# Kernel tuning notes

Measured on AMD Instinct MI355X. Metric: run time of the kernel, lower is better.

## Reference

```python
import jax, jax.numpy as jnp
import numpy as np

EPS = 1e-06
TOP_K = 2


def setup_inputs() -> dict:
    key = jax.random.key(0)
    k1, k2 = jax.random.split(key)
    B, S, H, E = 4, 4096, 2048, 64
    x = jax.random.normal(k1, (B, S, H), dtype=jnp.float32)
    per_dim_scale = jnp.ones((H,), dtype=jnp.float32)
    W = jax.random.normal(k2, (H, E), dtype=jnp.float32) * 0.02  # Dense kernel [H, E]
    return {"x": x, "per_dim_scale": per_dim_scale, "W": W}


def reference(x, per_dim_scale, W):
    H = x.shape[-1]
    x_flat = x.reshape(-1, H)  # [T, H]
    # Parameter-free RMSNorm (Gemma4VNorm)
    normed = x_flat * jax.lax.rsqrt(jnp.mean(jnp.square(x_flat), axis=-1, keepdims=True) + EPS)
    # scale by 1/sqrt(H), then learnable per-dim scale
    normed = normed * jnp.asarray(H, normed.dtype) ** -0.5
    normed = normed * per_dim_scale.astype(normed.dtype)
    router_logits = normed @ W  # [T, E]
    router_probs = jax.nn.softmax(router_logits.astype(jnp.float32), axis=-1).astype(x.dtype)
    top_k_probs, top_k_indices = jax.lax.top_k(router_probs, TOP_K)  # [T, k]
    denom = jnp.maximum(jnp.sum(top_k_probs, axis=-1, keepdims=True),
                        jnp.asarray(1e-09, top_k_probs.dtype))
    top_k_probs = top_k_probs / denom
    # Sparse dispatch weights [T, E] (sum of scaled one-hots == scatter-add)
    T = router_probs.shape[0]
    rows = jnp.arange(T)[:, None]  # [T, 1] broadcast against [T, k]
    dispatch_weights = jnp.zeros_like(router_probs).at[rows, top_k_indices].add(top_k_probs)
    return dispatch_weights
```

## Files before the change

kernel.cpp:

```cpp
#include <hip/hip_runtime.h>
#include <math.h>

#define H 2048
#define E 64
#define TAU 1e-6f

#define MT 16
#define NST 4

#define RB 16
#define CB 512
#define NCH (H / CB)
#define PITCH 516

#define WHI_OFF 65792u
#define WFRAG_BYTES 262144u
#define WLO_OFF (WHI_OFF + WFRAG_BYTES)
#define WS_NEEDED ((size_t)(WLO_OFF + WFRAG_BYTES))

typedef __attribute__((ext_vector_type(8))) short short8;
typedef __attribute__((ext_vector_type(4))) float f32x4;

__device__ __forceinline__ unsigned short bf16_rne(float f) {
    unsigned u = __float_as_uint(f);
    unsigned r = u + 0x7fffu + ((u >> 16) & 1u);
    return (unsigned short)(r >> 16);
}

__global__ __launch_bounds__(256)
void prep_w(const float* __restrict__ Wm, int* __restrict__ flags,
            unsigned short* __restrict__ whi, unsigned short* __restrict__ wlo)
{
    const int tid = blockIdx.x * 256 + threadIdx.x;
    if (tid == 0) flags[0] = 0;
    const int lane = tid & 63;
    const int fb   = tid >> 6;
    const int kc   = fb >> 2;
    const int n    = fb & 3;
    const int r0   = kc * 32 + (lane >> 4) * 8;
    const int col  = n * 16 + (lane & 15);

    short8 hv, lv;
#pragma unroll
    for (int j = 0; j < 8; ++j) {
        const float w = Wm[(r0 + j) * E + col];
        const unsigned short hb = bf16_rne(w);
        const float hf = __uint_as_float((unsigned)hb << 16);
        const unsigned short lb = bf16_rne(w - hf);
        hv[j] = (short)hb;
        lv[j] = (short)lb;
    }
    *(short8*)(whi + (size_t)tid * 8) = hv;
    *(short8*)(wlo + (size_t)tid * 8) = lv;
}

__global__ __launch_bounds__(256, 2)
void router_nb(const float* __restrict__ x,
               const float* __restrict__ pds,
               const unsigned short* __restrict__ whi,
               const unsigned short* __restrict__ wlo,
               float* __restrict__ out,
               int* __restrict__ flags)
{
    __shared__ __align__(16) unsigned short ybuf[4][2][4][520];
    __shared__ float ssbuf[64];
    __shared__ float sfac[16];

    const int t    = threadIdx.x;
    const int wid  = t >> 6;
    const int lane = t & 63;
    const int lgrp = lane >> 4;
    const int lsub = lane & 15;
    const int row0 = blockIdx.x * MT;

    const int kcl_w  = lsub >> 2;
    const int koff_w = (lsub & 3) * 8;
    const int kbase  = wid * 512;

    f32x4 acc[4] = {{0.f,0.f,0.f,0.f},{0.f,0.f,0.f,0.f},
                    {0.f,0.f,0.f,0.f},{0.f,0.f,0.f,0.f}};
    float sq[4] = {0.f, 0.f, 0.f, 0.f};

    float4 xv[4][2];
#pragma unroll
    for (int rr = 0; rr < 4; ++rr) {
        const float* p = x + (size_t)(row0 + rr * 4 + lgrp) * H + kbase + lsub * 8;
        xv[rr][0] = *(const float4*)p;
        xv[rr][1] = *(const float4*)(p + 4);
    }

    for (int st = 0; st < NST; ++st) {
        const float* pb = pds + kbase + st * 128 + lsub * 8;
        const float4 p0 = *(const float4*)pb;
        const float4 p1 = *(const float4*)(pb + 4);
#pragma unroll
        for (int rr = 0; rr < 4; ++rr) {
            const float4 a0 = xv[rr][0];
            const float4 a1 = xv[rr][1];
            sq[rr] += a0.x * a0.x + a0.y * a0.y + a0.z * a0.z + a0.w * a0.w
                    + a1.x * a1.x + a1.y * a1.y + a1.z * a1.z + a1.w * a1.w;
            const float y[8] = { a0.x * p0.x, a0.y * p0.y, a0.z * p0.z, a0.w * p0.w,
                                 a1.x * p1.x, a1.y * p1.y, a1.z * p1.z, a1.w * p1.w };
            short8 hv, lv;
#pragma unroll
            for (int e = 0; e < 8; ++e) {
                const unsigned short hb = bf16_rne(y[e]);
                const unsigned short lb = bf16_rne(y[e] - __uint_as_float((unsigned)hb << 16));
                hv[e] = (short)hb;
                lv[e] = (short)lb;
            }
            const int didx = (rr * 4 + lgrp) * 32 + koff_w;
            *(short8*)(&ybuf[wid][0][kcl_w][didx]) = hv;
            *(short8*)(&ybuf[wid][1][kcl_w][didx]) = lv;
        }

        if (st + 1 < NST) {
#pragma unroll
            for (int rr = 0; rr < 4; ++rr) {
                const float* p = x + (size_t)(row0 + rr * 4 + lgrp) * H
                               + kbase + (st + 1) * 128 + lsub * 8;
                xv[rr][0] = *(const float4*)p;
                xv[rr][1] = *(const float4*)(p + 4);
            }
        }

        const int aoff = lsub * 32 + lgrp * 8;
#pragma unroll
        for (int kcl = 0; kcl < 4; ++kcl) {
            const int kc = wid * 16 + st * 4 + kcl;
            const unsigned short* wbh = whi + (size_t)kc * 2048 + lane * 8;
            const unsigned short* wbl = wlo + (size_t)kc * 2048 + lane * 8;
            short8 bh[4], bl[4];
#pragma unroll
            for (int n = 0; n < 4; ++n) {
                bh[n] = *(const short8*)(wbh + n * 512);
                bl[n] = *(const short8*)(wbl + n * 512);
            }
            const short8 ah = *(const short8*)(&ybuf[wid][0][kcl][aoff]);
            const short8 al = *(const short8*)(&ybuf[wid][1][kcl][aoff]);
#pragma unroll
            for (int n = 0; n < 4; ++n) {
                acc[n] = __builtin_amdgcn_mfma_f32_16x16x32_bf16(ah, bh[n], acc[n], 0, 0, 0);
                acc[n] = __builtin_amdgcn_mfma_f32_16x16x32_bf16(ah, bl[n], acc[n], 0, 0, 0);
                acc[n] = __builtin_amdgcn_mfma_f32_16x16x32_bf16(al, bh[n], acc[n], 0, 0, 0);
            }
        }
    }

    float* lb = (float*)ybuf;
    float* lw = lb + wid * 2080;
#pragma unroll
    for (int n = 0; n < 4; ++n)
#pragma unroll
        for (int q = 0; q < 4; ++q)
            lw[(lgrp * 4 + q) * 64 + n * 16 + lsub] = acc[n][q];

#pragma unroll
    for (int rr = 0; rr < 4; ++rr) {
        float s = sq[rr];
        s += __shfl_xor(s, 1);
        s += __shfl_xor(s, 2);
        s += __shfl_xor(s, 4);
        s += __shfl_xor(s, 8);
        if (lsub == 0) ssbuf[wid * 16 + rr * 4 + lgrp] = s;
    }
    __syncthreads();

    if (t < 16) {
        const float tot = ssbuf[t] + ssbuf[16 + t] + ssbuf[32 + t] + ssbuf[48 + t];
        sfac[t] = rsqrtf(tot * (1.0f / (float)H) + 1e-6f) * 0.022097086912079608f;
    }
    __syncthreads();

#pragma unroll
    for (int rr = 0; rr < 4; ++rr) {
        const int r = wid * 4 + rr;
        const float L = (lb[r * 64 + lane]        + lb[2080 + r * 64 + lane]
                       + lb[4160 + r * 64 + lane] + lb[6240 + r * 64 + lane]) * sfac[r];

        float m = L;
#pragma unroll
        for (int off = 32; off >= 1; off >>= 1)
            m = fmaxf(m, __shfl_xor(m, off));
        const float ev = expf(L - m);
        float S = ev;
#pragma unroll
        for (int off = 32; off >= 1; off >>= 1)
            S += __shfl_xor(S, off);
        const float p = ev / S;

        float v1 = p; int i1 = lane;
#pragma unroll
        for (int off = 32; off >= 1; off >>= 1) {
            const float ov = __shfl_xor(v1, off);
            const int   oi = __shfl_xor(i1, off);
            if (ov > v1 || (ov == v1 && oi < i1)) { v1 = ov; i1 = oi; }
        }
        float v2 = (lane == i1) ? -1.0f : p; int i2 = lane;
#pragma unroll
        for (int off = 32; off >= 1; off >>= 1) {
            const float ov = __shfl_xor(v2, off);
            const int   oi = __shfl_xor(i2, off);
            if (ov > v2 || (ov == v2 && oi < i2)) { v2 = ov; i2 = oi; }
        }
        float v3 = (lane == i1 || lane == i2) ? -1.0f : p;
#pragma unroll
        for (int off = 32; off >= 1; off >>= 1)
            v3 = fmaxf(v3, __shfl_xor(v3, off));

        if (lane == 0 && (v2 - v3) < TAU) {
            const int k = atomicAdd(flags, 1);
            flags[1 + k] = row0 + r;
        }

        const float denom = fmaxf(v1 + v2, 1e-9f);
        const float wA = v1 / denom;
        const float wB = v2 / denom;
        const float o  = (lane == i1) ? wA : ((lane == i2) ? wB : 0.0f);
        out[(size_t)(row0 + r) * E + lane] = o;
    }
}

__global__ __launch_bounds__(256)
void router_fix(const float* __restrict__ x,
                const float* __restrict__ pds,
                const float* __restrict__ Wm,
                float* __restrict__ out,
                const int* __restrict__ flags)
{
    __shared__ double yd[H];
    __shared__ double parts[4 * E];
    __shared__ double ss[256];

    const int t = threadIdx.x;
    const int count = flags[0];

    for (int j = blockIdx.x; j < count; j += gridDim.x) {
        const int r = flags[1 + j];
        const float* xr = x + (size_t)r * H;

        double s = 0.0;
#pragma unroll
        for (int i = 0; i < 8; ++i) {
            const int h = t * 8 + i;
            const double xv = (double)xr[h];
            s += xv * xv;
            yd[h] = xv * (double)pds[h];
        }
        ss[t] = s;
        __syncthreads();

        const int ex = t & 63;
        const int sl = t >> 6;
        const float* wp = Wm + (size_t)(sl * 512) * E + ex;
        double acc = 0.0;
#pragma unroll 8
        for (int h = 0; h < 512; ++h)
            acc = fma(yd[sl * 512 + h], (double)wp[(size_t)h * E], acc);
        parts[sl * E + ex] = acc;
        __syncthreads();

        if (t < 64) {
            const int lane = t;
            double tot = ss[lane * 4] + ss[lane * 4 + 1] + ss[lane * 4 + 2] + ss[lane * 4 + 3];
#pragma unroll
            for (int off = 32; off >= 1; off >>= 1)
                tot += __shfl_xor(tot, off);
            const double sf = (1.0 / sqrt(tot * (1.0 / (double)H) + 1e-6)) * 0.022097086912079608;

            const double Ld = parts[0 * E + lane] + parts[1 * E + lane]
                            + parts[2 * E + lane] + parts[3 * E + lane];
            const float L = (float)(Ld * sf);

            float m = L;
#pragma unroll
            for (int off = 32; off >= 1; off >>= 1)
                m = fmaxf(m, __shfl_xor(m, off));
            const float ev = (float)exp((double)(L - m));
            float S = ev;
#pragma unroll
            for (int off = 32; off >= 1; off >>= 1)
                S += __shfl_xor(S, off);
            const float p = ev / S;

            float v1 = p; int i1 = lane;
#pragma unroll
            for (int off = 32; off >= 1; off >>= 1) {
                const float ov = __shfl_xor(v1, off);
                const int   oi = __shfl_xor(i1, off);
                if (ov > v1 || (ov == v1 && oi < i1)) { v1 = ov; i1 = oi; }
            }
            float v2 = (lane == i1) ? -1.0f : p; int i2 = lane;
#pragma unroll
            for (int off = 32; off >= 1; off >>= 1) {
                const float ov = __shfl_xor(v2, off);
                const int   oi = __shfl_xor(i2, off);
                if (ov > v2 || (ov == v2 && oi < i2)) { v2 = ov; i2 = oi; }
            }

            const float denom = fmaxf(v1 + v2, 1e-9f);
            const float wA = v1 / denom;
            const float wB = v2 / denom;
            const float o  = (lane == i1) ? wA : ((lane == i2) ? wB : 0.0f);
            out[(size_t)r * E + lane] = o;
        }
        __syncthreads();
    }
}

__global__ void zero_cnt(int* __restrict__ flags) {
    if (threadIdx.x == 0 && blockIdx.x == 0) flags[0] = 0;
}

__global__ __launch_bounds__(256)
void router_f32(const float* __restrict__ x,
                const float* __restrict__ pds,
                const float* __restrict__ Wm,
                float* __restrict__ out,
                int* __restrict__ flags)
{
    __shared__ __align__(16) float yb[RB * PITCH];
    __shared__ float ssbuf[256];
    __shared__ float sfac[RB];

    const int t    = threadIdx.x;
    const int wv_i = t >> 6;
    const int lane = t & 63;
    const int g    = lane >> 4;
    const int e0   = (lane & 15) << 2;

    const int row0 = blockIdx.x * RB;
    const int srow = t >> 4;
    const int sseg = t & 15;

    const float* xrow = x + (size_t)(row0 + srow) * H;

    float acc[4][4];
#pragma unroll
    for (int a = 0; a < 4; ++a)
#pragma unroll
        for (int b = 0; b < 4; ++b) acc[a][b] = 0.0f;

    float sumsq = 0.0f;
    float4 xv[8];
#pragma unroll
    for (int i = 0; i < 8; ++i)
        xv[i] = *(const float4*)(xrow + sseg * 4 + i * 64);

    for (int c = 0; c < NCH; ++c) {
        const float* pbase = pds + c * CB;
#pragma unroll
        for (int i = 0; i < 8; ++i) {
            const int hl = sseg * 4 + i * 64;
            const float4 a4 = xv[i];
            const float4 p4 = *(const float4*)(pbase + hl);
            sumsq += a4.x * a4.x + a4.y * a4.y + a4.z * a4.z + a4.w * a4.w;
            float4 y4;
            y4.x = a4.x * p4.x; y4.y = a4.y * p4.y;
            y4.z = a4.z * p4.z; y4.w = a4.w * p4.w;
            *(float4*)(&yb[srow * PITCH + hl]) = y4;
        }
        __syncthreads();

        if (c + 1 < NCH) {
            const int h0n = (c + 1) * CB;
#pragma unroll
            for (int i = 0; i < 8; ++i)
                xv[i] = *(const float4*)(xrow + h0n + sseg * 4 + i * 64);
        }

        const int hb = wv_i * 128;
        const float* wbase = Wm + (size_t)(c * CB) * E + e0;
#pragma unroll 2
        for (int s = 0; s < 32; ++s) {
            const int hh = hb + s * 4;
            const float4 w0 = *(const float4*)(wbase + (size_t)(hh + 0) * E);
            const float4 w1 = *(const float4*)(wbase + (size_t)(hh + 1) * E);
            const float4 w2 = *(const float4*)(wbase + (size_t)(hh + 2) * E);
            const float4 w3 = *(const float4*)(wbase + (size_t)(hh + 3) * E);
#pragma unroll
            for (int rr = 0; rr < 4; ++rr) {
                const float4 y4 = *(const float4*)(&yb[(4 * rr + g) * PITCH + hh]);
                acc[rr][0] = fmaf(y4.w, w3.x, fmaf(y4.z, w2.x, fmaf(y4.y, w1.x, fmaf(y4.x, w0.x, acc[rr][0]))));
                acc[rr][1] = fmaf(y4.w, w3.y, fmaf(y4.z, w2.y, fmaf(y4.y, w1.y, fmaf(y4.x, w0.y, acc[rr][1]))));
                acc[rr][2] = fmaf(y4.w, w3.z, fmaf(y4.z, w2.z, fmaf(y4.y, w1.z, fmaf(y4.x, w0.z, acc[rr][2]))));
                acc[rr][3] = fmaf(y4.w, w3.w, fmaf(y4.z, w2.w, fmaf(y4.y, w1.w, fmaf(y4.x, w0.w, acc[rr][3]))));
            }
        }
        __syncthreads();
    }

    ssbuf[t] = sumsq;
    __syncthreads();
    if (t < RB) {
        float tot = 0.0f;
#pragma unroll
        for (int i = 0; i < 16; ++i) tot += ssbuf[t * 16 + i];
        sfac[t] = rsqrtf(tot * (1.0f / (float)H) + 1e-6f) * 0.022097086912079608f;
    }

#pragma unroll
    for (int rr = 0; rr < 4; ++rr) {
        const int r = 4 * rr + g;
        *(float4*)(&yb[((wv_i * RB) + r) * E + e0]) =
            make_float4(acc[rr][0], acc[rr][1], acc[rr][2], acc[rr][3]);
    }
    __syncthreads();

#pragma unroll
    for (int rr = 0; rr < 4; ++rr) {
        const int r = wv_i * 4 + rr;
        float L = yb[(0 * RB + r) * E + lane] + yb[(1 * RB + r) * E + lane]
                + yb[(2 * RB + r) * E + lane] + yb[(3 * RB + r) * E + lane];
        L *= sfac[r];

        float m = L;
#pragma unroll
        for (int off = 32; off >= 1; off >>= 1)
            m = fmaxf(m, __shfl_xor(m, off));
        const float ev = expf(L - m);
        float S = ev;
#pragma unroll
        for (int off = 32; off >= 1; off >>= 1)
            S += __shfl_xor(S, off);
        const float p = ev / S;

        float v1 = p; int i1 = lane;
#pragma unroll
        for (int off = 32; off >= 1; off >>= 1) {
            const float ov = __shfl_xor(v1, off);
            const int   oi = __shfl_xor(i1, off);
            if (ov > v1 || (ov == v1 && oi < i1)) { v1 = ov; i1 = oi; }
        }
        float v2 = (lane == i1) ? -1.0f : p; int i2 = lane;
#pragma unroll
        for (int off = 32; off >= 1; off >>= 1) {
            const float ov = __shfl_xor(v2, off);
            const int   oi = __shfl_xor(i2, off);
            if (ov > v2 || (ov == v2 && oi < i2)) { v2 = ov; i2 = oi; }
        }
        float v3 = (lane == i1 || lane == i2) ? -1.0f : p;
#pragma unroll
        for (int off = 32; off >= 1; off >>= 1)
            v3 = fmaxf(v3, __shfl_xor(v3, off));

        if (lane == 0 && (v2 - v3) < TAU) {
            const int k = atomicAdd(flags, 1);
            flags[1 + k] = row0 + r;
        }

        const float denom = fmaxf(v1 + v2, 1e-9f);
        const float wA = v1 / denom;
        const float wB = v2 / denom;
        const float o  = (lane == i1) ? wA : ((lane == i2) ? wB : 0.0f);
        out[(size_t)(row0 + r) * E + lane] = o;
    }
}

extern "C" void kernel_launch(void* const* d_in, const int* in_sizes, int n_in,
                              void* d_out, int out_size, void* d_ws, size_t ws_size,
                              hipStream_t stream) {
    const float* x   = (const float*)d_in[0];
    const float* pds = (const float*)d_in[1];
    const float* Wm  = (const float*)d_in[2];
    float* out = (float*)d_out;
    int* flags = (int*)d_ws;

    const int T = in_sizes[0] / H;

    if (ws_size >= WS_NEEDED) {
        unsigned short* whi = (unsigned short*)((char*)d_ws + WHI_OFF);
        unsigned short* wlo = (unsigned short*)((char*)d_ws + WLO_OFF);
        hipLaunchKernelGGL(prep_w,     dim3(64),     dim3(256), 0, stream, Wm, flags, whi, wlo);
        hipLaunchKernelGGL(router_nb,  dim3(T / MT), dim3(256), 0, stream, x, pds, whi, wlo, out, flags);
        hipLaunchKernelGGL(router_fix, dim3(128),    dim3(256), 0, stream, x, pds, Wm, out, flags);
    } else {
        hipLaunchKernelGGL(zero_cnt,   dim3(1),      dim3(64),  0, stream, flags);
        hipLaunchKernelGGL(router_f32, dim3(T / RB), dim3(256), 0, stream, x, pds, Wm, out, flags);
        hipLaunchKernelGGL(router_fix, dim3(128),    dim3(256), 0, stream, x, pds, Wm, out, flags);
    }
}
```

Before: 85.90 us.

## Fold per-dim scale into W and load x directly as MFMA A-fragments

The per-dim scale is now folded into W during the prep kernel, using double precision before the hi/lo bf16 split, so the main kernel no longer multiplies x by it. The main kernel reads x straight from global memory in the MFMA A-fragment layout and splits it to bf16 hi/lo in registers. This removes the LDS staging buffer, its write/read round trip and the explicit prefetch pipeline. The trade-off is that global x reads now stride across 16 rows per wave, giving less contiguous access. Occupancy is also lowered to one block per SIMD set, with no software prefetch.

```diff
diff --git a/kernel.cpp b/kernel.cpp
--- a/kernel.cpp
+++ b/kernel.cpp
@@ -6,7 +6,7 @@
 #define TAU 1e-6f
 
 #define MT 16
-#define NST 4
+#define KCW 16
 
 #define RB 16
 #define CB 512
@@ -27,143 +27,103 @@
     return (unsigned short)(r >> 16);
 }
 
-__global__ __launch_bounds__(256)
-void prep_w(const float* __restrict__ Wm, int* __restrict__ flags,
+__global__ __launch_bounds__(64)
+void prep_w(const float* __restrict__ Wm, const float* __restrict__ pds,
+            int* __restrict__ flags,
             unsigned short* __restrict__ whi, unsigned short* __restrict__ wlo)
 {
-    const int tid = blockIdx.x * 256 + threadIdx.x;
-    if (tid == 0) flags[0] = 0;
-    const int lane = tid & 63;
-    const int fb   = tid >> 6;
-    const int kc   = fb >> 2;
-    const int n    = fb & 3;
-    const int r0   = kc * 32 + (lane >> 4) * 8;
-    const int col  = n * 16 + (lane & 15);
+    const int fb   = blockIdx.x;
+    const int lane = threadIdx.x;
+    if (fb == 0 && lane == 0) flags[0] = 0;
+    const int kc  = fb >> 2;
+    const int n   = fb & 3;
+    const int r0  = kc * 32 + (lane >> 4) * 8;
+    const int col = n * 16 + (lane & 15);
 
     short8 hv, lv;
 #pragma unroll
     for (int j = 0; j < 8; ++j) {
-        const float w = Wm[(r0 + j) * E + col];
-        const unsigned short hb = bf16_rne(w);
-        const float hf = __uint_as_float((unsigned)hb << 16);
-        const unsigned short lb = bf16_rne(w - hf);
+        const int r = r0 + j;
+        const double w = (double)pds[r] * (double)Wm[r * E + col];
+        const unsigned short hb = bf16_rne((float)w);
+        const double hd = (double)__uint_as_float((unsigned)hb << 16);
+        const unsigned short lb = bf16_rne((float)(w - hd));
         hv[j] = (short)hb;
         lv[j] = (short)lb;
     }
-    *(short8*)(whi + (size_t)tid * 8) = hv;
-    *(short8*)(wlo + (size_t)tid * 8) = lv;
-}
-
-__global__ __launch_bounds__(256, 2)
-void router_nb(const float* __restrict__ x,
-               const float* __restrict__ pds,
+    const size_t off = ((size_t)fb * 64 + lane) * 8;
+    *(short8*)(whi + off) = hv;
+    *(short8*)(wlo + off) = lv;
+}
+
+__global__ __launch_bounds__(256, 1)
+void router_df(const float* __restrict__ x,
                const unsigned short* __restrict__ whi,
                const unsigned short* __restrict__ wlo,
                float* __restrict__ out,
                int* __restrict__ flags)
 {
-    __shared__ __align__(16) unsigned short ybuf[4][2][4][520];
+    __shared__ float lbuf[4][MT * E];
     __shared__ float ssbuf[64];
     __shared__ float sfac[16];
 
     const int t    = threadIdx.x;
     const int wid  = t >> 6;
     const int lane = t & 63;
+    const int lsub = lane & 15;
     const int lgrp = lane >> 4;
-    const int lsub = lane & 15;
     const int row0 = blockIdx.x * MT;
 
-    const int kcl_w  = lsub >> 2;
-    const int koff_w = (lsub & 3) * 8;
-    const int kbase  = wid * 512;
+    const float* xbase = x + (size_t)(row0 + lsub) * H + wid * 512 + lgrp * 8;
 
     f32x4 acc[4] = {{0.f,0.f,0.f,0.f},{0.f,0.f,0.f,0.f},
                     {0.f,0.f,0.f,0.f},{0.f,0.f,0.f,0.f}};
-    float sq[4] = {0.f, 0.f, 0.f, 0.f};
-
-    float4 xv[4][2];
-#pragma unroll
-    for (int rr = 0; rr < 4; ++rr) {
-        const float* p = x + (size_t)(row0 + rr * 4 + lgrp) * H + kbase + lsub * 8;
-        xv[rr][0] = *(const float4*)p;
-        xv[rr][1] = *(const float4*)(p + 4);
-    }
-
-    for (int st = 0; st < NST; ++st) {
-        const float* pb = pds + kbase + st * 128 + lsub * 8;
-        const float4 p0 = *(const float4*)pb;
-        const float4 p1 = *(const float4*)(pb + 4);
-#pragma unroll
-        for (int rr = 0; rr < 4; ++rr) {
-            const float4 a0 = xv[rr][0];
-            const float4 a1 = xv[rr][1];
-            sq[rr] += a0.x * a0.x + a0.y * a0.y + a0.z * a0.z + a0.w * a0.w
-                    + a1.x * a1.x + a1.y * a1.y + a1.z * a1.z + a1.w * a1.w;
-            const float y[8] = { a0.x * p0.x, a0.y * p0.y, a0.z * p0.z, a0.w * p0.w,
-                                 a1.x * p1.x, a1.y * p1.y, a1.z * p1.z, a1.w * p1.w };
-            short8 hv, lv;
-#pragma unroll
-            for (int e = 0; e < 8; ++e) {
-                const unsigned short hb = bf16_rne(y[e]);
-                const unsigned short lb = bf16_rne(y[e] - __uint_as_float((unsigned)hb << 16));
-                hv[e] = (short)hb;
-                lv[e] = (short)lb;
-            }
-            const int didx = (rr * 4 + lgrp) * 32 + koff_w;
-            *(short8*)(&ybuf[wid][0][kcl_w][didx]) = hv;
-            *(short8*)(&ybuf[wid][1][kcl_w][didx]) = lv;
-        }
-
-        if (st + 1 < NST) {
-#pragma unroll
-            for (int rr = 0; rr < 4; ++rr) {
-                const float* p = x + (size_t)(row0 + rr * 4 + lgrp) * H
-                               + kbase + (st + 1) * 128 + lsub * 8;
-                xv[rr][0] = *(const float4*)p;
-                xv[rr][1] = *(const float4*)(p + 4);
-            }
-        }
-
-        const int aoff = lsub * 32 + lgrp * 8;
-#pragma unroll
-        for (int kcl = 0; kcl < 4; ++kcl) {
-            const int kc = wid * 16 + st * 4 + kcl;
-            const unsigned short* wbh = whi + (size_t)kc * 2048 + lane * 8;
-            const unsigned short* wbl = wlo + (size_t)kc * 2048 + lane * 8;
-            short8 bh[4], bl[4];
-#pragma unroll
-            for (int n = 0; n < 4; ++n) {
-                bh[n] = *(const short8*)(wbh + n * 512);
-                bl[n] = *(const short8*)(wbl + n * 512);
-            }
-            const short8 ah = *(const short8*)(&ybuf[wid][0][kcl][aoff]);
-            const short8 al = *(const short8*)(&ybuf[wid][1][kcl][aoff]);
-#pragma unroll
-            for (int n = 0; n < 4; ++n) {
-                acc[n] = __builtin_amdgcn_mfma_f32_16x16x32_bf16(ah, bh[n], acc[n], 0, 0, 0);
-                acc[n] = __builtin_amdgcn_mfma_f32_16x16x32_bf16(ah, bl[n], acc[n], 0, 0, 0);
-                acc[n] = __builtin_amdgcn_mfma_f32_16x16x32_bf16(al, bh[n], acc[n], 0, 0, 0);
-            }
-        }
-    }
-
-    float* lb = (float*)ybuf;
-    float* lw = lb + wid * 2080;
+    float sq = 0.0f;
+
+    for (int kl = 0; kl < KCW; ++kl) {
+        const float4 a0 = *(const float4*)(xbase + kl * 32);
+        const float4 a1 = *(const float4*)(xbase + kl * 32 + 4);
+
+        const int kc = wid * KCW + kl;
+        const unsigned short* ph = whi + ((size_t)kc * 256 + lane) * 8;
+        const unsigned short* pl = wlo + ((size_t)kc * 256 + lane) * 8;
+        short8 bh[4], bl[4];
+#pragma unroll
+        for (int n = 0; n < 4; ++n) {
+            bh[n] = *(const short8*)(ph + n * 512);
+            bl[n] = *(const short8*)(pl + n * 512);
+        }
+
+        sq += a0.x * a0.x + a0.y * a0.y + a0.z * a0.z + a0.w * a0.w
+            + a1.x * a1.x + a1.y * a1.y + a1.z * a1.z + a1.w * a1.w;
+
+        const float xf[8] = { a0.x, a0.y, a0.z, a0.w, a1.x, a1.y, a1.z, a1.w };
+        short8 ah, al;
+#pragma unroll
+        for (int e = 0; e < 8; ++e) {
+            const unsigned short hb = bf16_rne(xf[e]);
+            const unsigned short lb = bf16_rne(xf[e] - __uint_as_float((unsigned)hb << 16));
+            ah[e] = (short)hb;
+            al[e] = (short)lb;
+        }
+
+#pragma unroll
+        for (int n = 0; n < 4; ++n) {
+            acc[n] = __builtin_amdgcn_mfma_f32_16x16x32_bf16(ah, bh[n], acc[n], 0, 0, 0);
+            acc[n] = __builtin_amdgcn_mfma_f32_16x16x32_bf16(ah, bl[n], acc[n], 0, 0, 0);
+            acc[n] = __builtin_amdgcn_mfma_f32_16x16x32_bf16(al, bh[n], acc[n], 0, 0, 0);
+        }
+    }
+
 #pragma unroll
     for (int n = 0; n < 4; ++n)
 #pragma unroll
         for (int q = 0; q < 4; ++q)
-            lw[(lgrp * 4 + q) * 64 + n * 16 + lsub] = acc[n][q];
-
-#pragma unroll
-    for (int rr = 0; rr < 4; ++rr) {
-        float s = sq[rr];
-        s += __shfl_xor(s, 1);
-        s += __shfl_xor(s, 2);
-        s += __shfl_xor(s, 4);
-        s += __shfl_xor(s, 8);
-        if (lsub == 0) ssbuf[wid * 16 + rr * 4 + lgrp] = s;
-    }
+            lbuf[wid][(lgrp * 4 + q) * E + n * 16 + lsub] = acc[n][q];
+
+    sq += __shfl_xor(sq, 16);
+    sq += __shfl_xor(sq, 32);
+    if (lane < 16) ssbuf[wid * 16 + lane] = sq;
     __syncthreads();
 
     if (t < 16) {
@@ -175,8 +135,8 @@
 #pragma unroll
     for (int rr = 0; rr < 4; ++rr) {
         const int r = wid * 4 + rr;
-        const float L = (lb[r * 64 + lane]        + lb[2080 + r * 64 + lane]
-                       + lb[4160 + r * 64 + lane] + lb[6240 + r * 64 + lane]) * sfac[r];
+        const float L = (lbuf[0][r * E + lane] + lbuf[1][r * E + lane]
+                       + lbuf[2][r * E + lane] + lbuf[3][r * E + lane]) * sfac[r];
 
         float m = L;
 #pragma unroll
@@ -471,8 +431,8 @@
     if (ws_size >= WS_NEEDED) {
         unsigned short* whi = (unsigned short*)((char*)d_ws + WHI_OFF);
         unsigned short* wlo = (unsigned short*)((char*)d_ws + WLO_OFF);
-        hipLaunchKernelGGL(prep_w,     dim3(64),     dim3(256), 0, stream, Wm, flags, whi, wlo);
-        hipLaunchKernelGGL(router_nb,  dim3(T / MT), dim3(256), 0, stream, x, pds, whi, wlo, out, flags);
+        hipLaunchKernelGGL(prep_w,     dim3(256),    dim3(64),  0, stream, Wm, pds, flags, whi, wlo);
+        hipLaunchKernelGGL(router_df,  dim3(T / MT), dim3(256), 0, stream, x, whi, wlo, out, flags);
         hipLaunchKernelGGL(router_fix, dim3(128),    dim3(256), 0, stream, x, pds, Wm, out, flags);
     } else {
         hipLaunchKernelGGL(zero_cnt,   dim3(1),      dim3(64),  0, stream, flags);
```

Measured after the change: 87.52 us. About the same (+1.9%).
